# Performance work log

Measured on AMD Instinct MI355X. Metric: run time of the kernel, lower is better.

## Reference

```python
import jax, jax.numpy as jnp
import numpy as np

EPS = 1e-8
LRELU_SLOPE = 0.2
ACT_GAIN = float(np.sqrt(2.0))  # def_gain for lrelu
GAIN = 1.0                      # forward default
CLAMP = 256.0


def setup_inputs() -> dict:
    key = jax.random.key(0)
    k1, k2 = jax.random.split(key)
    x = jax.random.normal(k1, (8, 128, 32, 32, 32), dtype=jnp.float32)
    weight = jax.random.normal(k2, (128, 128, 3, 3, 3), dtype=jnp.float32)
    bias = jnp.zeros((128,), dtype=jnp.float32)
    return {"x": x, "weight": weight, "bias": bias}


def _modulated_conv3d(x, weight, styles, padding, demodulate=True):
    # x: [B, Cin, D, H, W], weight: [Cout, Cin, kd, kh, kw], styles: [B, Cin]
    w = weight[None] * styles[:, None, :, None, None, None]  # [B, Cout, Cin, kd, kh, kw]
    if demodulate:
        dcoefs = jax.lax.rsqrt(jnp.sum(jnp.square(w), axis=(2, 3, 4, 5)) + EPS)  # [B, Cout]
        w = w * dcoefs[:, :, None, None, None, None]
    pad = [(padding, padding)] * 3

    def per_sample(xi, wi):
        # xi: [Cin, D, H, W], wi: [Cout, Cin, kd, kh, kw]
        return jax.lax.conv_general_dilated(
            xi[None], wi, window_strides=(1, 1, 1), padding=pad,
            dimension_numbers=("NCDHW", "OIDHW", "NCDHW"))[0]

    return jax.vmap(per_sample)(x, w)  # [B, Cout, D, H, W]


def reference(x, weight, bias):
    padding = weight.shape[-1] // 2
    styles = jnp.ones((x.shape[0], weight.shape[1]), dtype=x.dtype)
    y = _modulated_conv3d(x, weight, styles, padding)
    y = jax.nn.leaky_relu(y + bias[None, :, None, None, None], LRELU_SLOPE)
    # clamp_gain(act, act_gain*gain, 256*gain)
    return jnp.clip(y * (ACT_GAIN * GAIN), -CLAMP * GAIN, CLAMP * GAIN)
```

## Files before the change

kernel.cpp:

```cpp
#include <hip/hip_runtime.h>

typedef short bf16x8 __attribute__((ext_vector_type(8)));
typedef float f32x4  __attribute__((ext_vector_type(4)));
typedef unsigned short u16;

static __device__ __forceinline__ u16 f2bf(float f) {
    unsigned int u = __builtin_bit_cast(unsigned int, f);
    u += 0x7FFFu + ((u >> 16) & 1u);
    return (u16)(u >> 16);
}

static __device__ __forceinline__ void gload_lds16(const void* g, void* l) {
    __builtin_amdgcn_global_load_lds((const __attribute__((address_space(1))) void*)g,
                                     (__attribute__((address_space(3))) void*)l, 16, 0, 0);
}

__global__ __launch_bounds__(256) void prep_w_k(const float* __restrict__ w,
                                                u16* __restrict__ wn) {
    const int co = blockIdx.x;
    const int t  = threadIdx.x;
    const float* wc = w + co * 3456;
    float s = 0.f;
    for (int i = t; i < 3456; i += 256) { float v = wc[i]; s += v * v; }
#pragma unroll
    for (int off = 32; off; off >>= 1) s += __shfl_down(s, off);
    __shared__ float red[4];
    __shared__ float dsh;
    if ((t & 63) == 0) red[t >> 6] = s;
    __syncthreads();
    if (t == 0) dsh = rsqrtf(red[0] + red[1] + red[2] + red[3] + 1e-8f);
    __syncthreads();
    const float d = dsh;
    for (int i = t; i < 3456; i += 256) {
        int ci = i / 27, tap = i - ci * 27;
        float v = wc[i] * d;
        wn[((tap * 4 + (ci >> 5)) * 128 + co) * 32 + (ci & 31)] = f2bf(v);
    }
}

__global__ __launch_bounds__(256) void xpose_k(const float* __restrict__ x,
                                               u16* __restrict__ xt) {
    const int bid = blockIdx.x;
    const int b = bid >> 10, d = (bid >> 5) & 31, h = bid & 31;
    const int t = threadIdx.x;
    const int w = t & 31, cg = t >> 5;
    const int base_dhw = d * 1024 + h * 32 + w;
#pragma unroll
    for (int r = 0; r < 2; ++r) {
        int g = cg + r * 8;
        const float* src = x + ((size_t)(b * 128 + g * 8) << 15) + base_dhw;
        bf16x8 pk;
#pragma unroll
        for (int j = 0; j < 8; ++j) pk[j] = (short)f2bf(src[(size_t)j << 15]);
        *(bf16x8*)&xt[((size_t)((b * 16 + g) << 15) + base_dhw) * 8] = pk;
    }
}

#define KSX 1048576
#define KSW 4096
#define RB  12288
__global__ __launch_bounds__(512, 4) void conv_mx(
    const u16* __restrict__ wsb, const float* __restrict__ bias,
    float* __restrict__ out) {
    __shared__ __align__(16) u16 lds[3 * RB];
    const u16* xt = wsb + 524288;
    const u16* wn = wsb + 512;
    const u16* zp = wsb;

    const int t = threadIdx.x, lane = t & 63, wid = t >> 6;
    const int ll = lane & 15, g = lane >> 4;
    const int mslice = wid >> 1, ncol = wid & 1;

    int wg = ((blockIdx.x & 7) << 7) | (blockIdx.x >> 3);
    const int b = wg >> 7, dt = (wg >> 3) & 15, ht = wg & 7;
    const int d0 = dt * 2, h0 = ht * 4;

    const int pos0 = mslice * 64 + ll;
    const int xro = pos0 * 32 + ((g ^ ((pos0 >> 1) & 3)) * 8);
    const int co0 = ncol * 64 + ll;
    const int wro = co0 * 32 + ((g ^ ((co0 >> 1) & 3)) * 8);

    const int posA = wid * 32 + (lane >> 2);
    const int slot = lane & 3;
    const int pdA = posA >> 7, phA = (posA >> 5) & 3, wA = posA & 31;
    const int gA = slot ^ ((posA >> 1) & 3);
    const int wco = wid * 16 + (lane >> 2);
    const u16* wsrc = wn + wco * 32 + ((slot ^ ((wco >> 1) & 3)) * 8);

    f32x4 acc[4][4];
#pragma unroll
    for (int i = 0; i < 4; ++i)
#pragma unroll
        for (int j = 0; j < 4; ++j) acc[i][j] = (f32x4){0.f, 0.f, 0.f, 0.f};

    int od_s = 0, oh_s = 0, ow_s = 0, cc_s = 0;
    const u16* xsA = xt; bool okA = false, okB = false;

#define DO_STAGE(SB) { \
    if (cc_s == 0) { \
        int Dx = d0 + pdA - 1 + od_s, Hx = h0 + phA - 1 + oh_s, Wx = wA - 1 + ow_s; \
        bool dh_ = ((unsigned)Dx < 32u) && ((unsigned)Hx < 32u); \
        okA = dh_ && ((unsigned)Wx < 32u); \
        okB = dh_ && (Wx < 16); \
        xsA = xt + (long)((b * 16 + gA) * 32768 + Dx * 1024 + Hx * 32 + Wx) * 8; } \
    gload_lds16(okA ? (const void*)xsA : (const void*)zp, (void*)&lds[(SB)*RB + wid*1024]); \
    gload_lds16(okB ? (const void*)(xsA + 128) : (const void*)zp, (void*)&lds[(SB)*RB + wid*1024 + 512]); \
    gload_lds16((const void*)wsrc, (void*)&lds[(SB)*RB + 8192 + wid*512]); \
    xsA += KSX; wsrc += KSW; \
    if (++cc_s == 4) { cc_s = 0; \
        if (++ow_s == 3) { ow_s = 0; if (++oh_s == 3) { oh_s = 0; ++od_s; } } } }

#define KSTEP(CB, SB, VMN, DOST) { \
    asm volatile("s_waitcnt vmcnt(" #VMN ")" ::: "memory"); \
    asm volatile("s_barrier" ::: "memory"); \
    bf16x8 xf[4], wf[4]; \
    _Pragma("unroll") for (int mf = 0; mf < 4; ++mf) \
        xf[mf] = *(const bf16x8*)&lds[(CB)*RB + xro + mf*512]; \
    _Pragma("unroll") for (int nf = 0; nf < 4; ++nf) \
        wf[nf] = *(const bf16x8*)&lds[(CB)*RB + 8192 + wro + nf*512]; \
    if (DOST) DO_STAGE(SB); \
    __builtin_amdgcn_s_setprio(1); \
    _Pragma("unroll") for (int mf = 0; mf < 4; ++mf) \
    _Pragma("unroll") for (int nf = 0; nf < 4; ++nf) \
        acc[mf][nf] = __builtin_amdgcn_mfma_f32_16x16x32_bf16(wf[nf], xf[mf], acc[mf][nf], 0, 0, 0); \
    __builtin_amdgcn_s_setprio(0); }

    DO_STAGE(0);
    DO_STAGE(1);

    for (int m = 0; m < 35; ++m) {
        KSTEP(0, 2, 3, 1);
        KSTEP(1, 0, 3, 1);
        KSTEP(2, 1, 3, 1);
    }
    KSTEP(0, 2, 3, 1);
    KSTEP(1, 0, 3, 0);
    KSTEP(2, 0, 0, 0);

    const int pd = mslice >> 1, phb = (mslice & 1) * 2;
#pragma unroll
    for (int nf = 0; nf < 4; ++nf) {
        f32x4 bb = *(const f32x4*)&bias[ncol * 64 + nf * 16 + g * 4];
#pragma unroll
        for (int mf = 0; mf < 4; ++mf) {
            const int wq = (mf & 1) * 16 + ll;
            const int hh = h0 + phb + (mf >> 1);
            float* orow = out + ((size_t)(b * 128 + ncol * 64 + nf * 16 + g * 4) << 15)
                          + (d0 + pd) * 1024 + hh * 32 + wq;
#pragma unroll
            for (int q = 0; q < 4; ++q) {
                float v = acc[mf][nf][q] + bb[q];
                v = v > 0.f ? v : v * 0.2f;
                v *= 1.41421356237f;
                v = fminf(fmaxf(v, -256.f), 256.f);
                orow[(size_t)q << 15] = v;
            }
        }
    }
#undef DO_STAGE
#undef KSTEP
}

#define NPOS 544
__global__ __launch_bounds__(256, 4) void conv_fb(
    const float* __restrict__ x, const u16* __restrict__ wn,
    const float* __restrict__ bias, float* __restrict__ out) {
    __shared__ __align__(16) u16 lds[NPOS * 32];
    float* ldsf = reinterpret_cast<float*>(lds);
    const int t = threadIdx.x;
    const int lane = t & 63;
    const int wid  = t >> 6;
    const int wr   = wid >> 1;
    const int wcn  = wid & 1;
    const int ll   = lane & 15;
    const int g    = lane >> 4;
    const int bid = blockIdx.x;
    const int b  = bid >> 8;
    const int dt = (bid >> 4) & 15, ht = bid & 15;
    const int d0 = dt * 2, h0 = ht * 2;
    const int sw  = t & 31;
    const int sg  = (t >> 5) & 3;
    const int rhi = t >> 7;
    f32x4 acc[4][4];
#pragma unroll
    for (int i = 0; i < 4; ++i)
#pragma unroll
        for (int j = 0; j < 4; ++j) acc[i][j] = (f32x4){0.f, 0.f, 0.f, 0.f};
    float bv[4][4];
#pragma unroll
    for (int nf = 0; nf < 4; ++nf) {
        f32x4 bb = *(const f32x4*)&bias[wcn * 64 + nf * 16 + g * 4];
#pragma unroll
        for (int q = 0; q < 4; ++q) bv[nf][q] = bb[q];
    }
    if (t < 128) {
        int pi  = t >> 2;
        int row = pi >> 1;
        int pos = row * 34 + (pi & 1) * 33;
        bf16x8 z = {0, 0, 0, 0, 0, 0, 0, 0};
        *(bf16x8*)&lds[pos * 32 + (t & 3) * 8] = z;
    }
    for (int c = 0; c < 4; ++c) {
        if (c) __syncthreads();
#pragma unroll
        for (int p = 0; p < 8; ++p) {
            int rowid = p * 2 + rhi;
            int pd = rowid >> 2, ph = rowid & 3;
            int d = d0 - 1 + pd, h = h0 - 1 + ph;
            bool ok = ((unsigned)d < 32u) && ((unsigned)h < 32u);
            const float* src = x + (((b * 128 + c * 32 + sg * 8) * 32 + d) * 32 + h) * 32 + sw;
            float v[8];
#pragma unroll
            for (int j = 0; j < 8; ++j) v[j] = ok ? src[j * 32768] : 0.f;
            bf16x8 pk;
#pragma unroll
            for (int j = 0; j < 8; ++j) pk[j] = (short)f2bf(v[j]);
            int pos = rowid * 34 + sw + 1;
            int sl = sg ^ ((pos >> 1) & 3);
            *(bf16x8*)&lds[pos * 32 + sl * 8] = pk;
        }
        __syncthreads();
        const u16* wbase = wn + c * 4096 + ((wcn * 64 + ll) * 32 + g * 8);
        bf16x8 wf[4];
#pragma unroll
        for (int nf = 0; nf < 4; ++nf) wf[nf] = *(const bf16x8*)&wbase[nf * 512];
#pragma unroll
        for (int tap = 0; tap < 27; ++tap) {
            const int od = tap / 9, oh = (tap / 3) % 3, ow = tap % 3;
            bf16x8 wfn[4];
            if (tap < 26) {
#pragma unroll
                for (int nf = 0; nf < 4; ++nf)
                    wfn[nf] = *(const bf16x8*)&wbase[(tap + 1) * 16384 + nf * 512];
            }
            bf16x8 xf[4];
#pragma unroll
            for (int mf = 0; mf < 4; ++mf) {
                int pos = ((wr + od) * 4 + (mf >> 1) + oh) * 34 + (mf & 1) * 16 + ll + ow;
                int sl = g ^ ((pos >> 1) & 3);
                xf[mf] = *(const bf16x8*)&lds[pos * 32 + sl * 8];
            }
            __builtin_amdgcn_s_setprio(1);
#pragma unroll
            for (int mf = 0; mf < 4; ++mf)
#pragma unroll
                for (int nf = 0; nf < 4; ++nf)
                    acc[mf][nf] = __builtin_amdgcn_mfma_f32_16x16x32_bf16(
                        wf[nf], xf[mf], acc[mf][nf], 0, 0, 0);
            __builtin_amdgcn_s_setprio(0);
            if (tap < 26) {
#pragma unroll
                for (int nf = 0; nf < 4; ++nf) wf[nf] = wfn[nf];
            }
        }
    }
#pragma unroll
    for (int p = 0; p < 4; ++p) {
        const int dd = p >> 1, hh = p & 1;
        __syncthreads();
        if (wr == dd) {
#pragma unroll
            for (int whalf = 0; whalf < 2; ++whalf) {
                const int mf = hh * 2 + whalf;
#pragma unroll
                for (int nf = 0; nf < 4; ++nf) {
#pragma unroll
                    for (int q = 0; q < 4; ++q) {
                        const int co = wcn * 64 + nf * 16 + g * 4 + q;
                        float v = acc[mf][nf][q] + bv[nf][q];
                        v = v > 0.f ? v : v * 0.2f;
                        v *= 1.41421356237f;
                        v = fminf(fmaxf(v, -256.f), 256.f);
                        ldsf[co * 33 + whalf * 16 + ll] = v;
                    }
                }
            }
        }
        __syncthreads();
#pragma unroll
        for (int it = 0; it < 4; ++it) {
            const int row = it * 32 + (t >> 3);
            const int ls  = t & 7;
            f32x4 v = *(f32x4*)&ldsf[row * 33 + ls * 4];
            *(f32x4*)&out[(size_t)(b * 128 + row) * 32768 +
                          (d0 + dd) * 1024 + (h0 + hh) * 32 + ls * 4] = v;
        }
    }
}

extern "C" void kernel_launch(void* const* d_in, const int* in_sizes, int n_in,
                              void* d_out, int out_size, void* d_ws, size_t ws_size,
                              hipStream_t stream) {
    const float* x    = (const float*)d_in[0];
    const float* w    = (const float*)d_in[1];
    const float* bias = (const float*)d_in[2];
    float* out        = (float*)d_out;
    u16* wsb          = (u16*)d_ws;

    hipMemsetAsync(d_ws, 0, 1024, stream);
    prep_w_k<<<128, 256, 0, stream>>>(w, wsb + 512);

    if (ws_size >= 68157440ull) {
        xpose_k<<<8192, 256, 0, stream>>>(x, wsb + 524288);
        conv_mx<<<1024, 512, 0, stream>>>(wsb, bias, out);
    } else {
        conv_fb<<<2048, 256, 0, stream>>>(x, wsb + 512, bias, out);
    }
}
```

Baseline: 296.2 us.

## Double the K-step per stage and split MFMA work into barrier-synced phases

Each LDS stage now holds two 32-channel K chunks, so the stage buffer doubles and occupancy drops from 4 to 2 blocks per CU. Every iteration runs four phases, each issuing 8 MFMAs for one M fragment, with LDS reads and global-to-LDS loads interleaved between barriers. The goal is to halve the number of pipeline iterations and overlap LDS reads and loads with MFMA execution more finely. In exchange it adds more barriers per iteration, and the lower occupancy leaves less latency hiding.

```diff
diff --git a/kernel.cpp b/kernel.cpp
--- a/kernel.cpp
+++ b/kernel.cpp
@@ -58,8 +58,8 @@
 
 #define KSX 1048576
 #define KSW 4096
-#define RB  12288
-__global__ __launch_bounds__(512, 4) void conv_mx(
+#define RB  24576
+__global__ __launch_bounds__(512, 2) void conv_p4(
     const u16* __restrict__ wsb, const float* __restrict__ bias,
     float* __restrict__ out) {
     __shared__ __align__(16) u16 lds[3 * RB];
@@ -78,7 +78,7 @@
     const int pos0 = mslice * 64 + ll;
     const int xro = pos0 * 32 + ((g ^ ((pos0 >> 1) & 3)) * 8);
     const int co0 = ncol * 64 + ll;
-    const int wro = co0 * 32 + ((g ^ ((co0 >> 1) & 3)) * 8);
+    const int wro = 16384 + co0 * 32 + ((g ^ ((co0 >> 1) & 3)) * 8);
 
     const int posA = wid * 32 + (lane >> 2);
     const int slot = lane & 3;
@@ -96,46 +96,72 @@
     int od_s = 0, oh_s = 0, ow_s = 0, cc_s = 0;
     const u16* xsA = xt; bool okA = false, okB = false;
 
-#define DO_STAGE(SB) { \
+#define DO_STAGE(SB, H) { \
     if (cc_s == 0) { \
         int Dx = d0 + pdA - 1 + od_s, Hx = h0 + phA - 1 + oh_s, Wx = wA - 1 + ow_s; \
         bool dh_ = ((unsigned)Dx < 32u) && ((unsigned)Hx < 32u); \
         okA = dh_ && ((unsigned)Wx < 32u); \
         okB = dh_ && (Wx < 16); \
         xsA = xt + (long)((b * 16 + gA) * 32768 + Dx * 1024 + Hx * 32 + Wx) * 8; } \
-    gload_lds16(okA ? (const void*)xsA : (const void*)zp, (void*)&lds[(SB)*RB + wid*1024]); \
-    gload_lds16(okB ? (const void*)(xsA + 128) : (const void*)zp, (void*)&lds[(SB)*RB + wid*1024 + 512]); \
-    gload_lds16((const void*)wsrc, (void*)&lds[(SB)*RB + 8192 + wid*512]); \
+    gload_lds16(okA ? (const void*)xsA : (const void*)zp, \
+                (void*)&lds[(SB)*RB + (H)*8192 + wid*1024]); \
+    gload_lds16(okB ? (const void*)(xsA + 128) : (const void*)zp, \
+                (void*)&lds[(SB)*RB + (H)*8192 + wid*1024 + 512]); \
+    gload_lds16((const void*)wsrc, \
+                (void*)&lds[(SB)*RB + 16384 + (H)*4096 + wid*512]); \
     xsA += KSX; wsrc += KSW; \
     if (++cc_s == 4) { cc_s = 0; \
         if (++ow_s == 3) { ow_s = 0; if (++oh_s == 3) { oh_s = 0; ++od_s; } } } }
 
-#define KSTEP(CB, SB, VMN, DOST) { \
-    asm volatile("s_waitcnt vmcnt(" #VMN ")" ::: "memory"); \
+#define MFMA8(P, XP) { \
+    __builtin_amdgcn_s_setprio(1); \
+    _Pragma("unroll") for (int nf = 0; nf < 4; ++nf) { \
+        acc[P][nf] = __builtin_amdgcn_mfma_f32_16x16x32_bf16(wf[nf][0], XP[0], acc[P][nf], 0, 0, 0); \
+        acc[P][nf] = __builtin_amdgcn_mfma_f32_16x16x32_bf16(wf[nf][1], XP[1], acc[P][nf], 0, 0, 0); } \
+    __builtin_amdgcn_s_setprio(0); }
+
+#define PH_SYNC() { \
+    asm volatile("s_waitcnt lgkmcnt(0)" ::: "memory"); \
+    asm volatile("s_barrier" ::: "memory"); }
+
+#define ITER(C, S, DOST, VM3) { \
+    bf16x8 wf[4][2], x0[2], x1[2], x2[2], x3[2]; \
+    _Pragma("unroll") for (int nf = 0; nf < 4; ++nf) { \
+        wf[nf][0] = *(const bf16x8*)&lds[(C)*RB + wro + nf * 512]; \
+        wf[nf][1] = *(const bf16x8*)&lds[(C)*RB + 4096 + wro + nf * 512]; } \
+    x0[0] = *(const bf16x8*)&lds[(C)*RB + xro]; \
+    x0[1] = *(const bf16x8*)&lds[(C)*RB + 8192 + xro]; \
+    if (DOST) DO_STAGE(S, 0); \
+    PH_SYNC(); \
+    MFMA8(0, x0); \
+    x1[0] = *(const bf16x8*)&lds[(C)*RB + xro + 512]; \
+    x1[1] = *(const bf16x8*)&lds[(C)*RB + 8192 + xro + 512]; \
+    if (DOST) DO_STAGE(S, 1); \
+    PH_SYNC(); \
+    MFMA8(1, x1); \
+    x2[0] = *(const bf16x8*)&lds[(C)*RB + xro + 1024]; \
+    x2[1] = *(const bf16x8*)&lds[(C)*RB + 8192 + xro + 1024]; \
+    PH_SYNC(); \
+    MFMA8(2, x2); \
+    x3[0] = *(const bf16x8*)&lds[(C)*RB + xro + 1536]; \
+    x3[1] = *(const bf16x8*)&lds[(C)*RB + 8192 + xro + 1536]; \
+    asm volatile("s_waitcnt lgkmcnt(0)" ::: "memory"); \
+    asm volatile("s_waitcnt " VM3 ::: "memory"); \
     asm volatile("s_barrier" ::: "memory"); \
-    bf16x8 xf[4], wf[4]; \
-    _Pragma("unroll") for (int mf = 0; mf < 4; ++mf) \
-        xf[mf] = *(const bf16x8*)&lds[(CB)*RB + xro + mf*512]; \
-    _Pragma("unroll") for (int nf = 0; nf < 4; ++nf) \
-        wf[nf] = *(const bf16x8*)&lds[(CB)*RB + 8192 + wro + nf*512]; \
-    if (DOST) DO_STAGE(SB); \
-    __builtin_amdgcn_s_setprio(1); \
-    _Pragma("unroll") for (int mf = 0; mf < 4; ++mf) \
-    _Pragma("unroll") for (int nf = 0; nf < 4; ++nf) \
-        acc[mf][nf] = __builtin_amdgcn_mfma_f32_16x16x32_bf16(wf[nf], xf[mf], acc[mf][nf], 0, 0, 0); \
-    __builtin_amdgcn_s_setprio(0); }
-
-    DO_STAGE(0);
-    DO_STAGE(1);
-
-    for (int m = 0; m < 35; ++m) {
-        KSTEP(0, 2, 3, 1);
-        KSTEP(1, 0, 3, 1);
-        KSTEP(2, 1, 3, 1);
-    }
-    KSTEP(0, 2, 3, 1);
-    KSTEP(1, 0, 3, 0);
-    KSTEP(2, 0, 0, 0);
+    MFMA8(3, x3); }
+
+    DO_STAGE(0, 0); DO_STAGE(0, 1); DO_STAGE(1, 0); DO_STAGE(1, 1);
+    asm volatile("s_waitcnt vmcnt(6)" ::: "memory");
+    asm volatile("s_barrier" ::: "memory");
+
+    for (int m = 0; m < 17; ++m) {
+        ITER(0, 2, 1, "vmcnt(6)");
+        ITER(1, 0, 1, "vmcnt(6)");
+        ITER(2, 1, 1, "vmcnt(6)");
+    }
+    ITER(0, 2, 1, "vmcnt(6)");
+    ITER(1, 0, 0, "vmcnt(0)");
+    ITER(2, 0, 0, "vmcnt(0)");
 
     const int pd = mslice >> 1, phb = (mslice & 1) * 2;
 #pragma unroll
@@ -158,7 +184,9 @@
         }
     }
 #undef DO_STAGE
-#undef KSTEP
+#undef MFMA8
+#undef PH_SYNC
+#undef ITER
 }
 
 #define NPOS 544
@@ -302,7 +330,7 @@
 
     if (ws_size >= 68157440ull) {
         xpose_k<<<8192, 256, 0, stream>>>(x, wsb + 524288);
-        conv_mx<<<1024, 512, 0, stream>>>(wsb, bias, out);
+        conv_p4<<<1024, 512, 0, stream>>>(wsb, bias, out);
     } else {
         conv_fb<<<2048, 256, 0, stream>>>(x, wsb + 512, bias, out);
     }
```

Result: no change. 294.7 us (-0.5%).
